# Optimization experiments

Hardware: AMD Instinct MI355X
Metric: run time of the kernel (lower is better)

## Reference

```python
import jax, jax.numpy as jnp
import numpy as np
import itertools

N_OBJECTS = 6  # subsets of range(6), sizes 1..6 -> 63 subsets

def _subset_groups():
    # group subsets by length so each group runs as one batched LSTM
    groups = {}
    for m in range(1, N_OBJECTS + 1):
        for s in itertools.combinations(range(6), m):
            groups.setdefault(m, []).append(list(s))
    return [(m, np.asarray(v, dtype=np.int32)) for m, v in groups.items()]

SUBSET_GROUPS = _subset_groups()


def _lstm_final_h(x, W_ih, W_hh, b_ih, b_hh):
    """x: [B,T,D] -> final hidden state [B,H]. PyTorch gate order i,f,g,o."""
    H = W_hh.shape[1]
    B = x.shape[0]
    # precompute input projections for all timesteps: [B,T,4H]
    xz = jnp.einsum('btd,gd->btg', x, W_ih) + b_ih + b_hh

    def step(carry, xt):
        h, c = carry
        z = xt + h @ W_hh.T
        i, f, g, o = jnp.split(z, 4, axis=-1)
        c = jax.nn.sigmoid(f) * c + jax.nn.sigmoid(i) * jnp.tanh(g)
        h = jax.nn.sigmoid(o) * jnp.tanh(c)
        return (h, c), None

    h0 = jnp.zeros((B, H), x.dtype)
    (h, _), _ = jax.lax.scan(step, (h0, h0), jnp.swapaxes(xz, 0, 1))
    return h


def setup_inputs() -> dict:
    key = jax.random.key(0)
    ks = jax.random.split(key, 10)
    D, H, FC, A = 16, 128, 256, 10
    mb = 8192
    s = lambda k, shape, fan: jax.random.normal(k, shape, jnp.float32) * (1.0 / np.sqrt(fan))
    return {
        'x_input': jax.random.normal(ks[0], (mb, 6, D), jnp.float32),
        'W_ih': s(ks[1], (4 * H, D), D),
        'W_hh': s(ks[2], (4 * H, H), H),
        'b_ih': jnp.zeros((4 * H,), jnp.float32),
        'b_hh': jnp.zeros((4 * H,), jnp.float32),
        'fc1_W': s(ks[3], (FC, H), H),
        'fc1_b': jnp.zeros((FC,), jnp.float32),
        'fc2_W': s(ks[4], (A, FC), FC),
        'fc2_b': jnp.zeros((A,), jnp.float32),
    }


def reference(x_input, W_ih, W_hh, b_ih, b_hh, fc1_W, fc1_b, fc2_W, fc2_b):
    mb = x_input.shape[0]
    H = W_hh.shape[1]
    hs = []
    # subsets of the same length are batched into one LSTM pass (fused form of
    # the original 63-iteration python loop); aggregation is permutation-invariant
    for m, idx in SUBSET_GROUPS:
        nL = idx.shape[0]
        xg = x_input[:, idx, :]                       # [mb, nL, m, D] gather
        xg = xg.reshape(mb * nL, m, x_input.shape[-1])
        h = _lstm_final_h(xg, W_ih, W_hh, b_ih, b_hh)  # [mb*nL, H]
        hs.append(h.reshape(mb, nL, H))
    holder = jnp.concatenate(hs, axis=1)              # [mb, 63, H]
    x = jnp.max(holder, axis=1)                       # aggregate == 'max'
    x = jax.nn.relu(x @ fc1_W.T + fc1_b)
    x = x @ fc2_W.T + fc2_b
    return jax.nn.log_softmax(x, axis=-1)
```

## Files before the change

### kernel.cpp

```cpp
#include <hip/hip_runtime.h>
#include <hip/hip_bf16.h>

#define BLOCK   512
#define NSAMP   16
#define HDIM    128
#define DDIM    16
#define NOBJ    6
#define NSLOT   14

typedef __attribute__((ext_vector_type(8))) short bf16x8;
typedef __attribute__((ext_vector_type(4))) float f32x4;

constexpr int pc6(int m)  { int c = 0; for (int i = 0; i < 6; ++i) c += (m >> i) & 1; return c; }
constexpr int msb6(int m) { int b = -1; for (int i = 0; i < 6; ++i) if (m & (1 << i)) b = i; return b; }

struct PNode { int jo, ps, sl; bool bar; };
struct Plan2 { PNode nd[63]; int lvlStart[8]; };
constexpr Plan2 make_plan2() {
    Plan2 P{};
    int slotOf[64] = {};
    bool busy[NSLOT] = {};
    int k = 0;
    for (int d = 1; d <= 6; ++d) {
        P.lvlStart[d] = k;
        for (int M = 1; M < 64; ++M) {
            if (pc6(M) != d || msb6(M) != 5) continue;
            P.nd[k].jo = 5;
            P.nd[k].ps = (d == 1) ? -1 : slotOf[M & ~(1 << 5)];
            P.nd[k].sl = -1;
            P.nd[k].bar = false;
            ++k;
        }
        int pend[20] = {}; int np = 0;
        for (int M = 1; M < 64; ++M)
            if (pc6(M) == d && msb6(M) < 5) pend[np++] = M;
        int key[20] = {};
        for (int i = 0; i < np; ++i) {
            if (d == 1) { key[i] = 0; continue; }
            const int par = pend[i] & ~(1 << msb6(pend[i]));
            int c2 = 0;
            for (int j2 = 0; j2 < np; ++j2)
                if ((pend[j2] & ~(1 << msb6(pend[j2]))) == par) ++c2;
            key[i] = c2;
        }
        for (int a = 0; a < np; ++a)
            for (int b2 = a + 1; b2 < np; ++b2)
                if (key[b2] < key[a]) {
                    int tm = key[a]; key[a] = key[b2]; key[b2] = tm;
                    tm = pend[a]; pend[a] = pend[b2]; pend[b2] = tm;
                }
        bool placed[20] = {};
        int nplaced = 0;
        bool firstPhase = true;
        while (nplaced < np) {
            bool needBar = !firstPhase;
            bool any = false;
            for (int i = 0; i < np; ++i) {
                if (placed[i]) continue;
                int fs = -1;
                for (int s = 0; s < NSLOT; ++s) if (!busy[s]) { fs = s; break; }
                if (fs < 0) break;
                const int M = pend[i]; const int hi = msb6(M);
                busy[fs] = true; slotOf[M] = fs;
                P.nd[k].jo = hi;
                P.nd[k].ps = (d == 1) ? -1 : slotOf[M & ~(1 << hi)];
                P.nd[k].sl = fs;
                P.nd[k].bar = needBar; needBar = false;
                ++k; placed[i] = true; ++nplaced; any = true;
            }
            firstPhase = false;
            if (nplaced < np) {
                if (!any) break;
                for (int M = 1; M < 64; ++M) {
                    if (pc6(M) != d - 1 || msb6(M) >= 5) continue;
                    bool allp = true;
                    for (int i = 0; i < np; ++i)
                        if (!placed[i] &&
                            ((pend[i] & ~(1 << msb6(pend[i]))) == M)) allp = false;
                    if (allp) busy[slotOf[M]] = false;
                }
            }
        }
        for (int s = 0; s < NSLOT; ++s) busy[s] = false;
        for (int M = 1; M < 64; ++M)
            if (pc6(M) == d && msb6(M) < 5) busy[slotOf[M]] = true;
    }
    P.lvlStart[7] = k;
    return P;
}
constexpr Plan2 PL2 = make_plan2();
static_assert(PL2.lvlStart[7] == 63, "plan must cover all 63 nodes");

#define LOG2E   1.44269504f
#define TWOL2E  2.88539008f
#define SLOT_SH 2048

__device__ __forceinline__ unsigned short f2bf(float x) {
    union { float f; unsigned int u; } a; a.f = x;
    unsigned int r = (a.u + 0x7FFFu + ((a.u >> 16) & 1u)) >> 16;
    return (unsigned short)r;
}
__device__ __forceinline__ unsigned pk2(float a, float b) {
    union { __hip_bfloat162 h; unsigned u; } z;
    z.h = __float22bfloat162_rn(float2{a, b});
    return z.u;
}
__device__ __forceinline__ float bflo(unsigned p) {
    union { unsigned u; float f; } a; a.u = p << 16; return a.f;
}
__device__ __forceinline__ float bfhi(unsigned p) {
    union { unsigned u; float f; } a; a.u = p & 0xFFFF0000u; return a.f;
}


__global__ __launch_bounds__(BLOCK)
__attribute__((amdgpu_waves_per_eu(2, 2)))
void subset_lstm_xz_kernel(
    const float* __restrict__ x_input,
    const float* __restrict__ W_ih,
    const float* __restrict__ W_hh,
    const float* __restrict__ b_ih,
    const float* __restrict__ b_hh,
    const float* __restrict__ fc1_W,
    const float* __restrict__ fc1_b,
    const float* __restrict__ fc2_W,
    const float* __restrict__ fc2_b,
    float* __restrict__ out)
{
    __shared__ __align__(16) unsigned short hs [NSLOT * SLOT_SH];
    __shared__ __align__(16) unsigned short csb[NSLOT * SLOT_SH];
    __shared__ __align__(16) unsigned short xb[NOBJ * 4 * NSAMP * 8];
    float* s_maxh  = (float*)hs;
    float* s_fc1   = (float*)(hs + 4096);
    float* s_logit = (float*)xb;

    const int t      = threadIdx.x;
    const int w      = t >> 6;
    const int lane   = t & 63;
    const int quad   = lane >> 4;
    const int m16    = lane & 15;
    const int s_base = blockIdx.x * NSAMP;

    for (int idx = t; idx < NOBJ * 4 * NSAMP * 8; idx += BLOCK) {
        const int j = idx & 7, n = (idx >> 3) & 15, q = (idx >> 7) & 3, obj = idx >> 9;
        float v;
        if (q < 2) v = x_input[(s_base + n) * (NOBJ * DDIM) + obj * DDIM + q * 8 + j];
        else       v = (q == 2 && j == 0) ? 1.0f : 0.0f;
        xb[idx] = f2bf(v);
    }

    bf16x8 wf[4][4];
    #pragma unroll
    for (int g = 0; g < 4; ++g) {
        const float sc = (g == 2) ? TWOL2E : -LOG2E;
        const int grow = g * HDIM + w * 16 + m16;
        const float* whr = W_hh + grow * HDIM;
        #pragma unroll
        for (int q = 0; q < 4; ++q) {
            union { unsigned short u[8]; bf16x8 v; } pk;
            #pragma unroll
            for (int j = 0; j < 8; ++j)
                pk.u[j] = f2bf(sc * whr[q * 32 + quad * 8 + j]);
            wf[g][q] = pk.v;
        }
    }

    __syncthreads();

    f32x4 xz[NOBJ][4];
    {
        bf16x8 bfx[NOBJ];
        #pragma unroll
        for (int o = 0; o < NOBJ; ++o)
            bfx[o] = *(const bf16x8*)&xb[((o * 4 + quad) * NSAMP + m16) * 8];
        const f32x4 fz = {0.f, 0.f, 0.f, 0.f};
        #pragma unroll
        for (int g = 0; g < 4; ++g) {
            const float sc = (g == 2) ? TWOL2E : -LOG2E;
            const int grow = g * HDIM + w * 16 + m16;
            const float* wir = W_ih + grow * DDIM;
            union { unsigned short u[8]; bf16x8 v; } pk;
            #pragma unroll
            for (int j = 0; j < 8; ++j) {
                float v = 0.0f;
                if (quad < 2) v = sc * wir[quad * 8 + j];
                else if (quad == 2 && j == 0) v = sc * (b_ih[grow] + b_hh[grow]);
                pk.u[j] = f2bf(v);
            }
            #pragma unroll
            for (int o = 0; o < NOBJ; ++o)
                xz[o][g] = __builtin_amdgcn_mfma_f32_16x16x32_bf16(
                    pk.v, bfx[o], fz, 0, 0, 0);
        }
    }

    float mh[4] = {-1e30f, -1e30f, -1e30f, -1e30f};
    const int kslot = w * 2 + (quad >> 1);
    unsigned short* const c_lane = &csb[(((w * 4 + quad) * NSAMP) + m16) * 4];

    #pragma unroll
    for (int d = 1; d <= 6; ++d) {
        __syncthreads();
        #pragma unroll
        for (int k = PL2.lvlStart[d]; k < PL2.lvlStart[d + 1]; ++k) {
            if (PL2.nd[k].bar) __syncthreads();
            const int jo = PL2.nd[k].jo;
            const int ps = PL2.nd[k].ps;
            const int sl = PL2.nd[k].sl;

            float cp[4] = {0.f, 0.f, 0.f, 0.f};
            f32x4 acc[4];
            if (ps >= 0) {
                const uint2 cpk = *(const uint2*)(c_lane + ps * SLOT_SH);
                cp[0] = bflo(cpk.x); cp[1] = bfhi(cpk.x);
                cp[2] = bflo(cpk.y); cp[3] = bfhi(cpk.y);
                {
                    const bf16x8 bh = *(const bf16x8*)
                        &hs[((ps * 16 + 0 * 4 + quad) * NSAMP + m16) * 8];
                    #pragma unroll
                    for (int g = 0; g < 4; ++g)
                        acc[g] = __builtin_amdgcn_mfma_f32_16x16x32_bf16(
                            wf[g][0], bh, xz[jo][g], 0, 0, 0);
                }
                #pragma unroll
                for (int q = 1; q < 4; ++q) {
                    const bf16x8 bh = *(const bf16x8*)
                        &hs[((ps * 16 + q * 4 + quad) * NSAMP + m16) * 8];
                    #pragma unroll
                    for (int g = 0; g < 4; ++g)
                        acc[g] = __builtin_amdgcn_mfma_f32_16x16x32_bf16(
                            wf[g][q], bh, acc[g], 0, 0, 0);
                }
            } else {
                #pragma unroll
                for (int g = 0; g < 4; ++g) acc[g] = xz[jo][g];
            }

            float cn4[4], hn4[4];
            #pragma unroll
            for (int r = 0; r < 4; ++r) {
                const float u  = 1.0f + __builtin_amdgcn_exp2f(acc[0][r]);
                const float q  = 1.0f + __builtin_amdgcn_exp2f(acc[1][r]);
                const float v  = 1.0f + __builtin_amdgcn_exp2f(acc[2][r]);
                const float qo = 1.0f + __builtin_amdgcn_exp2f(acc[3][r]);
                const float uv  = u * v;
                const float num = fmaf(q, v - 2.0f, cp[r] * uv);
                const float cn  = num * __builtin_amdgcn_rcpf(q * uv);
                const float wt  = 1.0f + __builtin_amdgcn_exp2f(TWOL2E * cn);
                const float h   = (wt - 2.0f) * __builtin_amdgcn_rcpf(qo * wt);
                cn4[r] = cn; hn4[r] = h;
                mh[r] = fmaxf(mh[r], h);
            }

            if (sl >= 0) {
                uint2 cw; cw.x = pk2(cn4[0], cn4[1]); cw.y = pk2(cn4[2], cn4[3]);
                *(uint2*)(c_lane + sl * SLOT_SH) = cw;
                uint2 hw; hw.x = pk2(hn4[0], hn4[1]); hw.y = pk2(hn4[2], hn4[3]);
                *(uint2*)&hs[((sl * 16 + kslot) * NSAMP + m16) * 8
                             + (quad & 1) * 4] = hw;
            }
        }
    }

    __syncthreads();
    {
        float4 v; v.x = mh[0]; v.y = mh[1]; v.z = mh[2]; v.w = mh[3];
        *(float4*)&s_maxh[m16 * HDIM + w * 16 + quad * 4] = v;
    }
    __syncthreads();

    {
        const int f  = t & 255;
        const int sh = t >> 8;
        float a1[8];
        #pragma unroll
        for (int s = 0; s < 8; ++s) a1[s] = fc1_b[f];
        for (int k4 = 0; k4 < HDIM / 4; ++k4) {
            const float4 wv = *(const float4*)&fc1_W[f * HDIM + k4 * 4];
            #pragma unroll
            for (int s = 0; s < 8; ++s) {
                const float4 h4 = *(const float4*)&s_maxh[(sh * 8 + s) * HDIM + k4 * 4];
                a1[s] += wv.x * h4.x + wv.y * h4.y + wv.z * h4.z + wv.w * h4.w;
            }
        }
        #pragma unroll
        for (int s = 0; s < 8; ++s)
            s_fc1[(sh * 8 + s) * 256 + f] = fmaxf(a1[s], 0.0f);
    }
    __syncthreads();

    if (t < NSAMP * 10) {
        const int s = t / 10, a = t % 10;
        float acc2 = fc2_b[a];
        for (int f4 = 0; f4 < 256 / 4; ++f4) {
            const float4 wv = *(const float4*)&fc2_W[a * 256 + f4 * 4];
            const float4 v  = *(const float4*)&s_fc1[s * 256 + f4 * 4];
            acc2 += wv.x * v.x + wv.y * v.y + wv.z * v.z + wv.w * v.w;
        }
        s_logit[s * 10 + a] = acc2;
    }
    __syncthreads();

    if (t < NSAMP) {
        float m = -1e30f;
        #pragma unroll
        for (int a = 0; a < 10; ++a) m = fmaxf(m, s_logit[t * 10 + a]);
        float sum = 0.0f;
        #pragma unroll
        for (int a = 0; a < 10; ++a) sum += __expf(s_logit[t * 10 + a] - m);
        const float lse = m + __logf(sum);
        #pragma unroll
        for (int a = 0; a < 10; ++a)
            out[(s_base + t) * 10 + a] = s_logit[t * 10 + a] - lse;
    }
}

extern "C" void kernel_launch(void* const* d_in, const int* in_sizes, int n_in,
                              void* d_out, int out_size, void* d_ws, size_t ws_size,
                              hipStream_t stream)
{
    (void)d_ws; (void)ws_size; (void)n_in; (void)out_size;

    const float* x   = (const float*)d_in[0];
    const float* Wih = (const float*)d_in[1];
    const float* Whh = (const float*)d_in[2];
    const float* bih = (const float*)d_in[3];
    const float* bhh = (const float*)d_in[4];
    const float* f1w = (const float*)d_in[5];
    const float* f1b = (const float*)d_in[6];
    const float* f2w = (const float*)d_in[7];
    const float* f2b = (const float*)d_in[8];

    const int mb = in_sizes[0] / (NOBJ * DDIM);
    dim3 grid(mb / NSAMP), block(BLOCK);
    subset_lstm_xz_kernel<<<grid, block, 0, stream>>>(
        x, Wih, Whh, bih, bhh, f1w, f1b, f2w, f2b, (float*)d_out);
}
```

Measured before the change: 205.6 us.

## Software-pipeline LSTM nodes and recompute input projection per node

Skews the per-level node loop so each node's MFMA chain is issued before the previous node's pointwise gate math, letting matrix and vector work overlap. It drops the precomputed per-object input projections held in registers and instead folds the W_ih projection into each node's MFMA chain via a fifth weight fragment. The occupancy hint is relaxed to allow up to 4 waves per EU. This trades extra MFMAs per node for lower register pressure and overlap. Moving the pointwise step past the next node's barrier may also affect ordering of shared-memory writes.

```diff
diff --git a/kernel.cpp b/kernel.cpp
--- a/kernel.cpp
+++ b/kernel.cpp
@@ -114,8 +114,8 @@
 
 
 __global__ __launch_bounds__(BLOCK)
-__attribute__((amdgpu_waves_per_eu(2, 2)))
-void subset_lstm_xz_kernel(
+__attribute__((amdgpu_waves_per_eu(2, 4)))
+void subset_lstm_skew_kernel(
     const float* __restrict__ x_input,
     const float* __restrict__ W_ih,
     const float* __restrict__ W_hh,
@@ -149,12 +149,13 @@
         xb[idx] = f2bf(v);
     }
 
-    bf16x8 wf[4][4];
+    bf16x8 wf[4][5];
     #pragma unroll
     for (int g = 0; g < 4; ++g) {
         const float sc = (g == 2) ? TWOL2E : -LOG2E;
         const int grow = g * HDIM + w * 16 + m16;
         const float* whr = W_hh + grow * HDIM;
+        const float* wir = W_ih + grow * DDIM;
         #pragma unroll
         for (int q = 0; q < 4; ++q) {
             union { unsigned short u[8]; bf16x8 v; } pk;
@@ -163,22 +164,7 @@
                 pk.u[j] = f2bf(sc * whr[q * 32 + quad * 8 + j]);
             wf[g][q] = pk.v;
         }
-    }
-
-    __syncthreads();
-
-    f32x4 xz[NOBJ][4];
-    {
-        bf16x8 bfx[NOBJ];
-        #pragma unroll
-        for (int o = 0; o < NOBJ; ++o)
-            bfx[o] = *(const bf16x8*)&xb[((o * 4 + quad) * NSAMP + m16) * 8];
-        const f32x4 fz = {0.f, 0.f, 0.f, 0.f};
-        #pragma unroll
-        for (int g = 0; g < 4; ++g) {
-            const float sc = (g == 2) ? TWOL2E : -LOG2E;
-            const int grow = g * HDIM + w * 16 + m16;
-            const float* wir = W_ih + grow * DDIM;
+        {
             union { unsigned short u[8]; bf16x8 v; } pk;
             #pragma unroll
             for (int j = 0; j < 8; ++j) {
@@ -187,10 +173,7 @@
                 else if (quad == 2 && j == 0) v = sc * (b_ih[grow] + b_hh[grow]);
                 pk.u[j] = f2bf(v);
             }
-            #pragma unroll
-            for (int o = 0; o < NOBJ; ++o)
-                xz[o][g] = __builtin_amdgcn_mfma_f32_16x16x32_bf16(
-                    pk.v, bfx[o], fz, 0, 0, 0);
+            wf[g][4] = pk.v;
         }
     }
 
@@ -198,68 +181,72 @@
     const int kslot = w * 2 + (quad >> 1);
     unsigned short* const c_lane = &csb[(((w * 4 + quad) * NSAMP) + m16) * 4];
 
+    auto mfma_node = [&](f32x4 (&acc)[4], uint2& cpk, int jo, int ps) {
+        cpk.x = 0u; cpk.y = 0u;
+        if (ps >= 0) cpk = *(const uint2*)(c_lane + ps * SLOT_SH);
+        {
+            const bf16x8 bfx = *(const bf16x8*)&xb[((jo * 4 + quad) * NSAMP + m16) * 8];
+            #pragma unroll
+            for (int g = 0; g < 4; ++g)
+                acc[g] = __builtin_amdgcn_mfma_f32_16x16x32_bf16(
+                    wf[g][4], bfx, f32x4{0.f, 0.f, 0.f, 0.f}, 0, 0, 0);
+        }
+        if (ps >= 0) {
+            #pragma unroll
+            for (int q = 0; q < 4; ++q) {
+                const bf16x8 bh = *(const bf16x8*)
+                    &hs[((ps * 16 + q * 4 + quad) * NSAMP + m16) * 8];
+                #pragma unroll
+                for (int g = 0; g < 4; ++g)
+                    acc[g] = __builtin_amdgcn_mfma_f32_16x16x32_bf16(
+                        wf[g][q], bh, acc[g], 0, 0, 0);
+            }
+        }
+    };
+
+    auto pointwise_node = [&](const f32x4 (&acc)[4], uint2 cpk, int sl) {
+        float cn4[4], hn4[4];
+        #pragma unroll
+        for (int r = 0; r < 4; ++r) {
+            const unsigned p = (r < 2) ? cpk.x : cpk.y;
+            const float cprev = (r & 1) ? bfhi(p) : bflo(p);
+            const float u  = 1.0f + __builtin_amdgcn_exp2f(acc[0][r]);
+            const float q  = 1.0f + __builtin_amdgcn_exp2f(acc[1][r]);
+            const float v  = 1.0f + __builtin_amdgcn_exp2f(acc[2][r]);
+            const float qo = 1.0f + __builtin_amdgcn_exp2f(acc[3][r]);
+            const float uv  = u * v;
+            const float num = fmaf(q, v - 2.0f, cprev * uv);
+            const float cn  = num * __builtin_amdgcn_rcpf(q * uv);
+            const float wt  = 1.0f + __builtin_amdgcn_exp2f(TWOL2E * cn);
+            const float h   = (wt - 2.0f) * __builtin_amdgcn_rcpf(qo * wt);
+            cn4[r] = cn; hn4[r] = h;
+            mh[r] = fmaxf(mh[r], h);
+        }
+        if (sl >= 0) {
+            uint2 cw; cw.x = pk2(cn4[0], cn4[1]); cw.y = pk2(cn4[2], cn4[3]);
+            *(uint2*)(c_lane + sl * SLOT_SH) = cw;
+            uint2 hw; hw.x = pk2(hn4[0], hn4[1]); hw.y = pk2(hn4[2], hn4[3]);
+            *(uint2*)&hs[((sl * 16 + kslot) * NSAMP + m16) * 8 + (quad & 1) * 4] = hw;
+        }
+    };
+
     #pragma unroll
     for (int d = 1; d <= 6; ++d) {
         __syncthreads();
-        #pragma unroll
-        for (int k = PL2.lvlStart[d]; k < PL2.lvlStart[d + 1]; ++k) {
+        const int kBeg = PL2.lvlStart[d];
+        const int kEnd = PL2.lvlStart[d + 1];
+        f32x4 accP[2][4];
+        uint2 cpP[2];
+        #pragma unroll
+        for (int k = kBeg; k < kEnd; ++k) {
+            const int par = (k - kBeg) & 1;
             if (PL2.nd[k].bar) __syncthreads();
-            const int jo = PL2.nd[k].jo;
-            const int ps = PL2.nd[k].ps;
-            const int sl = PL2.nd[k].sl;
-
-            float cp[4] = {0.f, 0.f, 0.f, 0.f};
-            f32x4 acc[4];
-            if (ps >= 0) {
-                const uint2 cpk = *(const uint2*)(c_lane + ps * SLOT_SH);
-                cp[0] = bflo(cpk.x); cp[1] = bfhi(cpk.x);
-                cp[2] = bflo(cpk.y); cp[3] = bfhi(cpk.y);
-                {
-                    const bf16x8 bh = *(const bf16x8*)
-                        &hs[((ps * 16 + 0 * 4 + quad) * NSAMP + m16) * 8];
-                    #pragma unroll
-                    for (int g = 0; g < 4; ++g)
-                        acc[g] = __builtin_amdgcn_mfma_f32_16x16x32_bf16(
-                            wf[g][0], bh, xz[jo][g], 0, 0, 0);
-                }
-                #pragma unroll
-                for (int q = 1; q < 4; ++q) {
-                    const bf16x8 bh = *(const bf16x8*)
-                        &hs[((ps * 16 + q * 4 + quad) * NSAMP + m16) * 8];
-                    #pragma unroll
-                    for (int g = 0; g < 4; ++g)
-                        acc[g] = __builtin_amdgcn_mfma_f32_16x16x32_bf16(
-                            wf[g][q], bh, acc[g], 0, 0, 0);
-                }
-            } else {
-                #pragma unroll
-                for (int g = 0; g < 4; ++g) acc[g] = xz[jo][g];
-            }
-
-            float cn4[4], hn4[4];
-            #pragma unroll
-            for (int r = 0; r < 4; ++r) {
-                const float u  = 1.0f + __builtin_amdgcn_exp2f(acc[0][r]);
-                const float q  = 1.0f + __builtin_amdgcn_exp2f(acc[1][r]);
-                const float v  = 1.0f + __builtin_amdgcn_exp2f(acc[2][r]);
-                const float qo = 1.0f + __builtin_amdgcn_exp2f(acc[3][r]);
-                const float uv  = u * v;
-                const float num = fmaf(q, v - 2.0f, cp[r] * uv);
-                const float cn  = num * __builtin_amdgcn_rcpf(q * uv);
-                const float wt  = 1.0f + __builtin_amdgcn_exp2f(TWOL2E * cn);
-                const float h   = (wt - 2.0f) * __builtin_amdgcn_rcpf(qo * wt);
-                cn4[r] = cn; hn4[r] = h;
-                mh[r] = fmaxf(mh[r], h);
-            }
-
-            if (sl >= 0) {
-                uint2 cw; cw.x = pk2(cn4[0], cn4[1]); cw.y = pk2(cn4[2], cn4[3]);
-                *(uint2*)(c_lane + sl * SLOT_SH) = cw;
-                uint2 hw; hw.x = pk2(hn4[0], hn4[1]); hw.y = pk2(hn4[2], hn4[3]);
-                *(uint2*)&hs[((sl * 16 + kslot) * NSAMP + m16) * 8
-                             + (quad & 1) * 4] = hw;
-            }
-        }
+            mfma_node(accP[par], cpP[par], PL2.nd[k].jo, PL2.nd[k].ps);
+            if (k > kBeg)
+                pointwise_node(accP[par ^ 1], cpP[par ^ 1], PL2.nd[k - 1].sl);
+        }
+        const int lpar = (kEnd - 1 - kBeg) & 1;
+        pointwise_node(accP[lpar], cpP[lpar], PL2.nd[kEnd - 1].sl);
     }
 
     __syncthreads();
@@ -333,6 +320,6 @@
 
     const int mb = in_sizes[0] / (NOBJ * DDIM);
     dim3 grid(mb / NSAMP), block(BLOCK);
-    subset_lstm_xz_kernel<<<grid, block, 0, stream>>>(
+    subset_lstm_skew_kernel<<<grid, block, 0, stream>>>(
         x, Wih, Whh, bih, bhh, f1w, f1b, f2w, f2b, (float*)d_out);
 }
```

After: 194.8 us. 5.2% less time.
